# Optimization experiments

Measured on AMD Instinct MI355X. Metric: run time of the kernel, lower is better.

Reference implementation:

```python
import jax, jax.numpy as jnp
import numpy as np

# Neuron hyperparameters (mid-range of the optuna search space)
THRESHOLD = 1.0
CURRENT_DECAY = 0.3
VOLTAGE_DECAY = 0.8
TAU_GRAD = 0.5
SCALE_GRAD = 1.0

B, N_IN, H, N_OUT, T = 64, 2048, 1024, 2, 128
SPIKE_RATE = 0.1  # input spike density


@jax.custom_vjp
def spike_fn(v):
    # Heaviside spike with SLAYER exponential surrogate gradient
    return (v >= 0.0).astype(v.dtype)

def _spike_fwd(v):
    return spike_fn(v), v

def _spike_bwd(v, g):
    return (g * SCALE_GRAD * jnp.exp(-jnp.abs(v) / TAU_GRAD),)

spike_fn.defvjp(_spike_fwd, _spike_bwd)


def cuba_dense(spike, W):
    """One SLAYER CUBA Dense block: dense synapse + leaky IF neuron over time.
    spike: [B, N_in, T], W: [N_out, N_in] -> [B, N_out, T] output spikes."""
    z = jnp.einsum('oi,bit->tbo', W, spike)  # synaptic current input, [T, B, O]
    O = W.shape[0]
    zeros = jnp.zeros((spike.shape[0], O), spike.dtype)

    def step(carry, z_t):
        cur, vol = carry
        cur = cur * (1.0 - CURRENT_DECAY) + z_t          # current dynamics
        vol = vol * (1.0 - VOLTAGE_DECAY) + cur          # voltage dynamics
        s = spike_fn(vol - THRESHOLD)                    # threshold spike
        vol = vol * (1.0 - s)                            # reset to zero on spike
        return (cur, vol), s

    _, s = jax.lax.scan(step, (zeros, zeros), z)
    return jnp.transpose(s, (1, 2, 0))  # [B, O, T]


def setup_inputs() -> dict:
    key = jax.random.key(0)
    k0, k1, k2, k3 = jax.random.split(key, 4)
    spike = (jax.random.uniform(k0, (B, N_IN, T)) < SPIKE_RATE).astype(jnp.float32)
    W1 = jax.random.normal(k1, (H, N_IN), jnp.float32) / np.sqrt(N_IN).astype(np.float32)
    W2 = jax.random.normal(k2, (H, H), jnp.float32) / np.sqrt(H).astype(np.float32)
    W3 = jax.random.normal(k3, (N_OUT, H), jnp.float32) / np.sqrt(H).astype(np.float32)
    return {"spike": spike, "W1": W1, "W2": W2, "W3": W3}


def reference(spike, W1, W2, W3):
    s = cuba_dense(spike, W1)
    s = cuba_dense(s, W2)
    s = cuba_dense(s, W3)
    return s  # [B, 2, T]
```

## Files before the change

kernel.cpp:

```cpp
#include <hip/hip_runtime.h>


typedef unsigned short ushort_t;
typedef unsigned int uint_t;
typedef __bf16 bf16x8 __attribute__((ext_vector_type(8)));
typedef float f32x4 __attribute__((ext_vector_type(4)));

#define O_TOT 1024

__device__ __forceinline__ void glds16(const ushort_t* g, ushort_t* l) {
  __builtin_amdgcn_global_load_lds(
      (const __attribute__((address_space(1))) uint_t*)g,
      (__attribute__((address_space(3))) uint_t*)l, 16, 0, 0);
}

__device__ __forceinline__ ushort_t f32_to_bf16_rne(float f) {
  uint_t u = __float_as_uint(f);
  u += 0x7FFFu + ((u >> 16) & 1u);
  return (ushort_t)(u >> 16);
}

__global__ __launch_bounds__(256) void split_w(const float* __restrict__ W1,
                                               const float* __restrict__ W2,
                                               ushort_t* __restrict__ h1,
                                               ushort_t* __restrict__ l1,
                                               ushort_t* __restrict__ h2,
                                               ushort_t* __restrict__ l2) {
  int idx = blockIdx.x * 256 + threadIdx.x;
  const int N1 = 1024 * 2048;
  if (idx < N1) {
    float w = W1[idx];
    ushort_t h = f32_to_bf16_rne(w);
    h1[idx] = h;
    l1[idx] = f32_to_bf16_rne(w - __uint_as_float(((uint_t)h) << 16));
  } else {
    int k = idx - N1;
    float w = W2[k];
    ushort_t h = f32_to_bf16_rne(w);
    h2[k] = h;
    l2[k] = f32_to_bf16_rne(w - __uint_as_float(((uint_t)h) << 16));
  }
}

__global__ __launch_bounds__(256) void transpose_spike(const float* __restrict__ spike,
                                                       ushort_t* __restrict__ A1) {
  __shared__ ushort_t lds[32 * 130];
  const int tid = threadIdx.x;
  const int b = blockIdx.y;
  const int i0 = blockIdx.x * 32;
#pragma unroll
  for (int it = 0; it < 4; ++it) {
    int p = it * 256 + tid;
    int i = p >> 5, tg = (p & 31) * 4;
    float4 v = *(const float4*)(spike + ((size_t)b * 2048 + i0 + i) * 128 + tg);
    lds[i * 130 + tg + 0] = (v.x != 0.0f) ? 0x3F80u : 0u;
    lds[i * 130 + tg + 1] = (v.y != 0.0f) ? 0x3F80u : 0u;
    lds[i * 130 + tg + 2] = (v.z != 0.0f) ? 0x3F80u : 0u;
    lds[i * 130 + tg + 3] = (v.w != 0.0f) ? 0x3F80u : 0u;
  }
  __syncthreads();
  uint_t* A1u = (uint_t*)A1;
#pragma unroll
  for (int it = 0; it < 8; ++it) {
    int p = it * 256 + tid;
    int t = p >> 4, iu = p & 15;
    uint_t u = (uint_t)lds[(2 * iu) * 130 + t] | ((uint_t)lds[(2 * iu + 1) * 130 + t] << 16);
    A1u[((size_t)(b * 128 + t) * 2048 + i0) / 2 + iu] = u;
  }
}

__global__ __launch_bounds__(256, 4)
void gemm_scan(const ushort_t* __restrict__ A, const ushort_t* __restrict__ Bhi,
               const ushort_t* __restrict__ Blo, ushort_t* __restrict__ S,
               int K) {
  __shared__ float smemf[128 * 65];
  ushort_t* As = (ushort_t*)smemf;
  ushort_t* Bh = As + 8192;
  ushort_t* Bl = Bh + 4096;
  float* Zt = smemf;

  const int tid = threadIdx.x;
  const int wave = tid >> 6, lane = tid & 63;
  const int b = blockIdx.y;
  const int m0 = b * 128;
  const int o0 = blockIdx.x * 64;
  const int qm = wave >> 1, qn = wave & 1;
  const int fr = lane & 15, q = lane >> 4;

  f32x4 acc[4][2];
#pragma unroll
  for (int i = 0; i < 4; ++i)
#pragma unroll
    for (int j = 0; j < 2; ++j) acc[i][j] = (f32x4){0.f, 0.f, 0.f, 0.f};

  size_t gA[4];
  ushort_t* lA[4];
#pragma unroll
  for (int r = 0; r < 4; ++r) {
    int s = wave * 256 + r * 64 + lane;
    int row = s >> 3;
    int u = (s & 7) ^ (row & 7);
    gA[r] = (size_t)(m0 + row) * K + u * 8;
    lA[r] = As + (size_t)(wave * 256 + r * 64) * 8;
  }
  size_t gB[2];
  ushort_t *lBh[2], *lBl[2];
#pragma unroll
  for (int r = 0; r < 2; ++r) {
    int s = wave * 128 + r * 64 + lane;
    int row = s >> 3;
    int u = (s & 7) ^ (row & 7);
    gB[r] = (size_t)(o0 + row) * K + u * 8;
    lBh[r] = Bh + (size_t)(wave * 128 + r * 64) * 8;
    lBl[r] = Bl + (size_t)(wave * 128 + r * 64) * 8;
  }

  int aoff[4][2], boff[2][2];
#pragma unroll
  for (int i = 0; i < 4; ++i)
#pragma unroll
    for (int kk = 0; kk < 2; ++kk) {
      int row = qm * 64 + i * 16 + fr;
      int u = (kk * 4 + q) ^ (row & 7);
      aoff[i][kk] = row * 64 + u * 8;
    }
#pragma unroll
  for (int j = 0; j < 2; ++j)
#pragma unroll
    for (int kk = 0; kk < 2; ++kk) {
      int row = qn * 32 + j * 16 + fr;
      int u = (kk * 4 + q) ^ (row & 7);
      boff[j][kk] = row * 64 + u * 8;
    }

  for (int kc = 0; kc < K; kc += 64) {
#pragma unroll
    for (int r = 0; r < 4; ++r) glds16(A + gA[r] + kc, lA[r]);
#pragma unroll
    for (int r = 0; r < 2; ++r) {
      glds16(Bhi + gB[r] + kc, lBh[r]);
      glds16(Blo + gB[r] + kc, lBl[r]);
    }
    __syncthreads();

#pragma unroll
    for (int kk = 0; kk < 2; ++kk) {
      bf16x8 af[4], bh[2], bl[2];
#pragma unroll
      for (int i = 0; i < 4; ++i) af[i] = *(const bf16x8*)(As + aoff[i][kk]);
#pragma unroll
      for (int j = 0; j < 2; ++j) {
        bh[j] = *(const bf16x8*)(Bh + boff[j][kk]);
        bl[j] = *(const bf16x8*)(Bl + boff[j][kk]);
      }
#pragma unroll
      for (int i = 0; i < 4; ++i)
#pragma unroll
        for (int j = 0; j < 2; ++j) {
          acc[i][j] = __builtin_amdgcn_mfma_f32_16x16x32_bf16(af[i], bh[j], acc[i][j], 0, 0, 0);
          acc[i][j] = __builtin_amdgcn_mfma_f32_16x16x32_bf16(af[i], bl[j], acc[i][j], 0, 0, 0);
        }
    }
    __syncthreads();
  }

#pragma unroll
  for (int i = 0; i < 4; ++i)
#pragma unroll
    for (int j = 0; j < 2; ++j)
#pragma unroll
      for (int rr = 0; rr < 4; ++rr)
        Zt[(qm * 64 + i * 16 + q * 4 + rr) * 65 + qn * 32 + j * 16 + fr] = acc[i][j][rr];
  __syncthreads();

  if (tid < 64) {
#pragma clang fp contract(off)
    float cur = 0.0f, vol = 0.0f;
    const int o = o0 + tid;
    for (int t = 0; t < 128; ++t) {
      float z = Zt[t * 65 + tid];
      cur = cur * 0.7f;
      cur = cur + z;
      vol = vol * 0.2f;
      vol = vol + cur;
      float v = vol - 1.0f;
      float s = (v >= 0.0f) ? 1.0f : 0.0f;
      vol = vol * (1.0f - s);
      S[(size_t)(m0 + t) * O_TOT + o] = (v >= 0.0f) ? 0x3F80u : 0u;
    }
  }
}

__global__ __launch_bounds__(256) void gemm3_scan(const ushort_t* __restrict__ X,
                                                  const float* __restrict__ W3,
                                                  float* __restrict__ out) {
  __shared__ float w3s[2048];
  __shared__ float z3[256];
  __shared__ float sp[256];
  const int tid = threadIdx.x;
  const int b = blockIdx.x;
  for (int i = tid; i < 2048; i += 256) w3s[i] = W3[i];
  __syncthreads();
  const int wave = tid >> 6, lane = tid & 63;
  for (int tt = 0; tt < 32; ++tt) {
    int t = wave * 32 + tt;
    const uint_t* row = (const uint_t*)(X + (size_t)(b * 128 + t) * 1024) + lane * 8;
    float s0 = 0.0f, s1 = 0.0f;
#pragma unroll
    for (int jw = 0; jw < 8; ++jw) {
      uint_t u = row[jw];
      float x0 = __uint_as_float(u << 16);
      float x1 = __uint_as_float(u & 0xFFFF0000u);
      int i0 = lane * 16 + jw * 2;
      s0 = fmaf(x0, w3s[i0], s0);
      s1 = fmaf(x0, w3s[1024 + i0], s1);
      s0 = fmaf(x1, w3s[i0 + 1], s0);
      s1 = fmaf(x1, w3s[1024 + i0 + 1], s1);
    }
#pragma unroll
    for (int off = 32; off > 0; off >>= 1) {
      s0 += __shfl_down(s0, off);
      s1 += __shfl_down(s1, off);
    }
    if (lane == 0) {
      z3[t * 2] = s0;
      z3[t * 2 + 1] = s1;
    }
  }
  __syncthreads();
  if (tid < 2) {
#pragma clang fp contract(off)
    float cur = 0.0f, vol = 0.0f;
    for (int t = 0; t < 128; ++t) {
      float z = z3[t * 2 + tid];
      cur = cur * 0.7f;
      cur = cur + z;
      vol = vol * 0.2f;
      vol = vol + cur;
      float v = vol - 1.0f;
      float s = (v >= 0.0f) ? 1.0f : 0.0f;
      vol = vol * (1.0f - s);
      sp[tid * 128 + t] = s;
    }
  }
  __syncthreads();
  out[b * 256 + tid] = sp[tid];
}

extern "C" void kernel_launch(void* const* d_in, const int* in_sizes, int n_in,
                              void* d_out, int out_size, void* d_ws, size_t ws_size,
                              hipStream_t stream) {
  const float* spike = (const float*)d_in[0];
  const float* W1 = (const float*)d_in[1];
  const float* W2 = (const float*)d_in[2];
  const float* W3 = (const float*)d_in[3];
  float* out = (float*)d_out;

  char* ws = (char*)d_ws;
  ushort_t* A1 = (ushort_t*)ws;
  ushort_t* S2 = (ushort_t*)(ws + (size_t)32 * 1024 * 1024);
  ushort_t* S3 = (ushort_t*)(ws + (size_t)48 * 1024 * 1024);
  ushort_t* W1hi = (ushort_t*)(ws + (size_t)64 * 1024 * 1024);
  ushort_t* W1lo = (ushort_t*)(ws + (size_t)68 * 1024 * 1024);
  ushort_t* W2hi = (ushort_t*)(ws + (size_t)72 * 1024 * 1024);
  ushort_t* W2lo = (ushort_t*)(ws + (size_t)74 * 1024 * 1024);

  split_w<<<12288, 256, 0, stream>>>(W1, W2, W1hi, W1lo, W2hi, W2lo);
  transpose_spike<<<dim3(64, 64), 256, 0, stream>>>(spike, A1);
  gemm_scan<<<dim3(16, 64), 256, 0, stream>>>(A1, W1hi, W1lo, S2, 2048);
  gemm_scan<<<dim3(16, 64), 256, 0, stream>>>(S2, W2hi, W2lo, S3, 1024);
  gemm3_scan<<<64, 256, 0, stream>>>(S3, W3, out);
}
```

Before: 241.7 us.

## Use 32x32 MFMA, prefetch next K tile during compute, merge prep kernels

The GEMM loop now loads all fragments for a K-chunk into registers, syncs, then issues async global-to-LDS loads for the next chunk before running the MFMAs, so memory traffic overlaps with compute in a single LDS buffer. The MFMA shape moves from 16x16x32 to 32x32x16, which halves the instruction count per tile and reuses A/B fragments more. The weight split and spike transpose kernels are merged into one launch. The added register pressure from holding all fragments may lower occupancy.

```diff
diff --git a/kernel.cpp b/kernel.cpp
--- a/kernel.cpp
+++ b/kernel.cpp
@@ -4,7 +4,7 @@
 typedef unsigned short ushort_t;
 typedef unsigned int uint_t;
 typedef __bf16 bf16x8 __attribute__((ext_vector_type(8)));
-typedef float f32x4 __attribute__((ext_vector_type(4)));
+typedef float f32x16 __attribute__((ext_vector_type(16)));
 
 #define O_TOT 1024
 
@@ -20,34 +20,36 @@
   return (ushort_t)(u >> 16);
 }
 
-__global__ __launch_bounds__(256) void split_w(const float* __restrict__ W1,
-                                               const float* __restrict__ W2,
-                                               ushort_t* __restrict__ h1,
-                                               ushort_t* __restrict__ l1,
-                                               ushort_t* __restrict__ h2,
-                                               ushort_t* __restrict__ l2) {
-  int idx = blockIdx.x * 256 + threadIdx.x;
-  const int N1 = 1024 * 2048;
-  if (idx < N1) {
-    float w = W1[idx];
-    ushort_t h = f32_to_bf16_rne(w);
-    h1[idx] = h;
-    l1[idx] = f32_to_bf16_rne(w - __uint_as_float(((uint_t)h) << 16));
-  } else {
-    int k = idx - N1;
-    float w = W2[k];
-    ushort_t h = f32_to_bf16_rne(w);
-    h2[k] = h;
-    l2[k] = f32_to_bf16_rne(w - __uint_as_float(((uint_t)h) << 16));
-  }
-}
-
-__global__ __launch_bounds__(256) void transpose_spike(const float* __restrict__ spike,
-                                                       ushort_t* __restrict__ A1) {
+__global__ __launch_bounds__(256) void prep(const float* __restrict__ W1,
+                                            const float* __restrict__ W2,
+                                            const float* __restrict__ spike,
+                                            ushort_t* __restrict__ h1,
+                                            ushort_t* __restrict__ l1,
+                                            ushort_t* __restrict__ h2,
+                                            ushort_t* __restrict__ l2,
+                                            ushort_t* __restrict__ A1) {
+  const int tid = threadIdx.x;
+  if (blockIdx.x < 12288) {
+    int idx = blockIdx.x * 256 + tid;
+    const int N1 = 1024 * 2048;
+    if (idx < N1) {
+      float w = W1[idx];
+      ushort_t h = f32_to_bf16_rne(w);
+      h1[idx] = h;
+      l1[idx] = f32_to_bf16_rne(w - __uint_as_float(((uint_t)h) << 16));
+    } else {
+      int k = idx - N1;
+      float w = W2[k];
+      ushort_t h = f32_to_bf16_rne(w);
+      h2[k] = h;
+      l2[k] = f32_to_bf16_rne(w - __uint_as_float(((uint_t)h) << 16));
+    }
+    return;
+  }
   __shared__ ushort_t lds[32 * 130];
-  const int tid = threadIdx.x;
-  const int b = blockIdx.y;
-  const int i0 = blockIdx.x * 32;
+  const int bid = blockIdx.x - 12288;
+  const int b = bid >> 6;
+  const int i0 = (bid & 63) * 32;
 #pragma unroll
   for (int it = 0; it < 4; ++it) {
     int p = it * 256 + tid;
@@ -85,13 +87,13 @@
   const int m0 = b * 128;
   const int o0 = blockIdx.x * 64;
   const int qm = wave >> 1, qn = wave & 1;
-  const int fr = lane & 15, q = lane >> 4;
-
-  f32x4 acc[4][2];
-#pragma unroll
-  for (int i = 0; i < 4; ++i)
-#pragma unroll
-    for (int j = 0; j < 2; ++j) acc[i][j] = (f32x4){0.f, 0.f, 0.f, 0.f};
+  const int r32 = lane & 31, h = lane >> 5;
+
+  f32x16 acc[2];
+#pragma unroll
+  for (int i = 0; i < 2; ++i)
+#pragma unroll
+    for (int r = 0; r < 16; ++r) acc[i][r] = 0.0f;
 
   size_t gA[4];
   ushort_t* lA[4];
@@ -115,62 +117,69 @@
     lBl[r] = Bl + (size_t)(wave * 128 + r * 64) * 8;
   }
 
-  int aoff[4][2], boff[2][2];
-#pragma unroll
-  for (int i = 0; i < 4; ++i)
-#pragma unroll
-    for (int kk = 0; kk < 2; ++kk) {
-      int row = qm * 64 + i * 16 + fr;
-      int u = (kk * 4 + q) ^ (row & 7);
-      aoff[i][kk] = row * 64 + u * 8;
-    }
-#pragma unroll
-  for (int j = 0; j < 2; ++j)
-#pragma unroll
-    for (int kk = 0; kk < 2; ++kk) {
-      int row = qn * 32 + j * 16 + fr;
-      int u = (kk * 4 + q) ^ (row & 7);
-      boff[j][kk] = row * 64 + u * 8;
-    }
+  int aoff[2][4], boff[4];
+#pragma unroll
+  for (int i = 0; i < 2; ++i) {
+    int row = qm * 64 + i * 32 + r32;
+#pragma unroll
+    for (int s = 0; s < 4; ++s) aoff[i][s] = row * 64 + ((s * 2 + h) ^ (row & 7)) * 8;
+  }
+  {
+    int row = qn * 32 + r32;
+#pragma unroll
+    for (int s = 0; s < 4; ++s) boff[s] = row * 64 + ((s * 2 + h) ^ (row & 7)) * 8;
+  }
+
+#pragma unroll
+  for (int r = 0; r < 4; ++r) glds16(A + gA[r], lA[r]);
+#pragma unroll
+  for (int r = 0; r < 2; ++r) {
+    glds16(Bhi + gB[r], lBh[r]);
+    glds16(Blo + gB[r], lBl[r]);
+  }
+  __syncthreads();
 
   for (int kc = 0; kc < K; kc += 64) {
-#pragma unroll
-    for (int r = 0; r < 4; ++r) glds16(A + gA[r] + kc, lA[r]);
-#pragma unroll
-    for (int r = 0; r < 2; ++r) {
-      glds16(Bhi + gB[r] + kc, lBh[r]);
-      glds16(Blo + gB[r] + kc, lBl[r]);
+    bf16x8 af[2][4], bh[4], bl[4];
+#pragma unroll
+    for (int i = 0; i < 2; ++i)
+#pragma unroll
+      for (int s = 0; s < 4; ++s) af[i][s] = *(const bf16x8*)(As + aoff[i][s]);
+#pragma unroll
+    for (int s = 0; s < 4; ++s) {
+      bh[s] = *(const bf16x8*)(Bh + boff[s]);
+      bl[s] = *(const bf16x8*)(Bl + boff[s]);
     }
     __syncthreads();
 
-#pragma unroll
-    for (int kk = 0; kk < 2; ++kk) {
-      bf16x8 af[4], bh[2], bl[2];
-#pragma unroll
-      for (int i = 0; i < 4; ++i) af[i] = *(const bf16x8*)(As + aoff[i][kk]);
-#pragma unroll
-      for (int j = 0; j < 2; ++j) {
-        bh[j] = *(const bf16x8*)(Bh + boff[j][kk]);
-        bl[j] = *(const bf16x8*)(Bl + boff[j][kk]);
+    if (kc + 64 < K) {
+      int kn = kc + 64;
+#pragma unroll
+      for (int r = 0; r < 4; ++r) glds16(A + gA[r] + kn, lA[r]);
+#pragma unroll
+      for (int r = 0; r < 2; ++r) {
+        glds16(Bhi + gB[r] + kn, lBh[r]);
+        glds16(Blo + gB[r] + kn, lBl[r]);
       }
-#pragma unroll
-      for (int i = 0; i < 4; ++i)
-#pragma unroll
-        for (int j = 0; j < 2; ++j) {
-          acc[i][j] = __builtin_amdgcn_mfma_f32_16x16x32_bf16(af[i], bh[j], acc[i][j], 0, 0, 0);
-          acc[i][j] = __builtin_amdgcn_mfma_f32_16x16x32_bf16(af[i], bl[j], acc[i][j], 0, 0, 0);
-        }
-    }
+    }
+
+#pragma unroll
+    for (int s = 0; s < 4; ++s)
+#pragma unroll
+      for (int i = 0; i < 2; ++i) {
+        acc[i] = __builtin_amdgcn_mfma_f32_32x32x16_bf16(af[i][s], bh[s], acc[i], 0, 0, 0);
+        acc[i] = __builtin_amdgcn_mfma_f32_32x32x16_bf16(af[i][s], bl[s], acc[i], 0, 0, 0);
+      }
     __syncthreads();
   }
 
 #pragma unroll
-  for (int i = 0; i < 4; ++i)
-#pragma unroll
-    for (int j = 0; j < 2; ++j)
-#pragma unroll
-      for (int rr = 0; rr < 4; ++rr)
-        Zt[(qm * 64 + i * 16 + q * 4 + rr) * 65 + qn * 32 + j * 16 + fr] = acc[i][j][rr];
+  for (int i = 0; i < 2; ++i)
+#pragma unroll
+    for (int reg = 0; reg < 16; ++reg) {
+      int t = qm * 64 + i * 32 + (reg & 3) + 8 * (reg >> 2) + 4 * h;
+      Zt[t * 65 + qn * 32 + r32] = acc[i][reg];
+    }
   __syncthreads();
 
   if (tid < 64) {
@@ -265,8 +274,7 @@
   ushort_t* W2hi = (ushort_t*)(ws + (size_t)72 * 1024 * 1024);
   ushort_t* W2lo = (ushort_t*)(ws + (size_t)74 * 1024 * 1024);
 
-  split_w<<<12288, 256, 0, stream>>>(W1, W2, W1hi, W1lo, W2hi, W2lo);
-  transpose_spike<<<dim3(64, 64), 256, 0, stream>>>(spike, A1);
+  prep<<<16384, 256, 0, stream>>>(W1, W2, spike, W1hi, W1lo, W2hi, W2lo, A1);
   gemm_scan<<<dim3(16, 64), 256, 0, stream>>>(A1, W1hi, W1lo, S2, 2048);
   gemm_scan<<<dim3(16, 64), 256, 0, stream>>>(S2, W2hi, W2lo, S3, 1024);
   gemm3_scan<<<64, 256, 0, stream>>>(S3, W3, out);
```

After: 263.4 us. +9.0%, slower.
